# Kernel tuning notes

Hardware: AMD Instinct MI355X
Metric: run time of the kernel (lower is better)

The kernel has to match this reference:

```python
import jax, jax.numpy as jnp
import numpy as np

E, H, HD = 2048, 32, 64
SCALE = HD ** -0.5


def setup_inputs() -> dict:
    key = jax.random.key(0)
    ks = jax.random.split(key, 11)
    B, T, P = 16, 4, 4096
    S = P + T
    return {
        "hidden_states": jax.random.normal(ks[0], (B, T, E), jnp.float32),
        "past_key": jax.random.normal(ks[1], (1, H, P, HD), jnp.float32),
        "past_value": jax.random.normal(ks[2], (1, H, P, HD), jnp.float32),
        "attention_mask": jnp.zeros((B, 1, T, S), jnp.float32),
        "Wq": jax.random.normal(ks[3], (E, E), jnp.float32) * 0.02,
        "bq": jax.random.normal(ks[4], (E,), jnp.float32) * 0.02,
        "Wk": jax.random.normal(ks[5], (E, E), jnp.float32) * 0.02,
        "bk": jax.random.normal(ks[6], (E,), jnp.float32) * 0.02,
        "Wv": jax.random.normal(ks[7], (E, E), jnp.float32) * 0.02,
        "bv": jax.random.normal(ks[8], (E,), jnp.float32) * 0.02,
        "Wo": jax.random.normal(ks[9], (E, E), jnp.float32) * 0.02,
        "bo": jax.random.normal(ks[10], (E,), jnp.float32) * 0.02,
    }


def _shape(x, B, S):
    # [B,S,E] -> [B,H,S,hd]
    return x.reshape(B, S, H, HD).transpose(0, 2, 1, 3)


def reference(hidden_states, past_key, past_value, attention_mask,
              Wq, bq, Wk, bk, Wv, bv, Wo, bo):
    B, T, _ = hidden_states.shape
    # projections (torch Linear: x @ W.T + b); query pre-scaled
    q = _shape(hidden_states @ Wq.T + bq, B, T) * SCALE   # [B,H,T,hd]
    k_new = _shape(hidden_states @ Wk.T + bk, B, T)       # [B,H,T,hd]
    v_new = _shape(hidden_states @ Wv.T + bv, B, T)
    # cache stored with batch 1, broadcast (torch repeat) to B, then concat
    k_past = jnp.broadcast_to(past_key, (B,) + past_key.shape[1:])
    v_past = jnp.broadcast_to(past_value, (B,) + past_value.shape[1:])
    k = jnp.concatenate([k_past, k_new], axis=2)          # [B,H,S,hd]
    v = jnp.concatenate([v_past, v_new], axis=2)
    scores = jnp.einsum('bhtd,bhsd->bhts', q, k)          # [B,H,T,S]
    scores = scores + attention_mask                      # mask is [B,1,T,S]
    scores = jnp.maximum(scores, jnp.finfo(scores.dtype).min)
    w = jax.nn.softmax(scores, axis=-1)
    out = jnp.einsum('bhts,bhsd->bhtd', w, v)             # [B,H,T,hd]
    out = out.transpose(0, 2, 1, 3).reshape(B, T, E)
    return out @ Wo.T + bo
```

## Files before the change

kernel.cpp:

```cpp
#include <hip/hip_runtime.h>


typedef float f4 __attribute__((ext_vector_type(4)));
typedef short s8v __attribute__((ext_vector_type(8)));

#define NEG_HUGE (-3.402823466e38f)

__device__ inline unsigned short f2bs(float x) {
  union { float f; unsigned int u; } a; a.f = x;
  unsigned int u = a.u;
  u += 0x7fffu + ((u >> 16) & 1u);
  return (unsigned short)(u >> 16);
}
__device__ inline float bs2f(unsigned short s) {
  union { unsigned int u; float f; } a; a.u = ((unsigned int)s) << 16;
  return a.f;
}
__device__ inline unsigned long long pack4(float a, float b, float c, float d) {
  return (unsigned long long)f2bs(a) | ((unsigned long long)f2bs(b) << 16)
       | ((unsigned long long)f2bs(c) << 32) | ((unsigned long long)f2bs(d) << 48);
}
__device__ inline s8v cvt8(f4 a, f4 b) {
  s8v r;
  r[0]=(short)f2bs(a[0]); r[1]=(short)f2bs(a[1]); r[2]=(short)f2bs(a[2]); r[3]=(short)f2bs(a[3]);
  r[4]=(short)f2bs(b[0]); r[5]=(short)f2bs(b[1]); r[6]=(short)f2bs(b[2]); r[7]=(short)f2bs(b[3]);
  return r;
}
__device__ inline f4 mfma16(s8v a, s8v b, f4 c) {
  return __builtin_amdgcn_mfma_f32_16x16x32_bf16(a, b, c, 0, 0, 0);
}
__device__ inline f4 fzero() { f4 z = {0.f,0.f,0.f,0.f}; return z; }
__device__ inline float wave_sum(float v) {
  #pragma unroll
  for (int off = 32; off; off >>= 1) v += __shfl_xor(v, off, 64);
  return v;
}

__global__ __launch_bounds__(256) void k_qkv(
    const float* __restrict__ hs, const float* __restrict__ Wq,
    const float* __restrict__ Wk, const float* __restrict__ Wv,
    float* __restrict__ part) {
  __shared__ __align__(16) unsigned short As[64 * 264];
  const int n0 = blockIdx.x * 64;
  const int ksb = blockIdx.y;
  const int p = n0 >> 11;
  const int c0 = n0 & 2047;
  const float* W = (p == 0) ? Wq : (p == 1) ? Wk : Wv;
  const int t = threadIdx.x, lane = t & 63, w = t >> 6;
  const int cl = lane & 15, quad = lane >> 4;

  f4 acc[4];
  #pragma unroll
  for (int i = 0; i < 4; ++i) acc[i] = fzero();

  const int cw = c0 + w * 16 + cl;
  for (int kt = 0; kt < 2; ++kt) {
    const int k0 = ksb * 512 + kt * 256;
    __syncthreads();
    #pragma unroll
    for (int i = 0; i < 16; ++i) {
      int idx4 = t + (i << 8);
      int row = idx4 >> 6;
      int col = (idx4 & 63) << 2;
      f4 v = *reinterpret_cast<const f4*>(hs + row * 2048 + k0 + col);
      *reinterpret_cast<unsigned long long*>(&As[row * 264 + col]) =
          pack4(v[0], v[1], v[2], v[3]);
    }
    __syncthreads();
    const float* wbase = W + (size_t)cw * 2048 + k0;
    #pragma unroll
    for (int ks2 = 0; ks2 < 8; ++ks2) {
      const int kb = ks2 * 32 + quad * 8;
      f4 w0 = *reinterpret_cast<const f4*>(wbase + kb);
      f4 w1 = *reinterpret_cast<const f4*>(wbase + kb + 4);
      s8v bf = cvt8(w0, w1);
      #pragma unroll
      for (int mt = 0; mt < 4; ++mt) {
        s8v af = *reinterpret_cast<const s8v*>(&As[(mt * 16 + cl) * 264 + kb]);
        acc[mt] = mfma16(af, bf, acc[mt]);
      }
    }
  }
  float* outp = part + (size_t)ksb * 64 * 6144;
  #pragma unroll
  for (int mt = 0; mt < 4; ++mt)
    #pragma unroll
    for (int rg = 0; rg < 4; ++rg) {
      int r = mt * 16 + quad * 4 + rg;
      outp[r * 6144 + n0 + w * 16 + cl] = acc[mt][rg];
    }
}

__global__ __launch_bounds__(256) void k_qkv_red(
    const float* __restrict__ part, const float* __restrict__ bq,
    const float* __restrict__ bk, const float* __restrict__ bv,
    unsigned short* __restrict__ qws, float* __restrict__ knew,
    float* __restrict__ vnew) {
  int idx = blockIdx.x * 256 + threadIdx.x;
  int r = idx / 6144;
  int n = idx - r * 6144;
  float s = part[idx] + part[idx + 393216] + part[idx + 786432] + part[idx + 1179648];
  int c = n & 2047, p = n >> 11;
  int h = c >> 6, d = c & 63;
  int b = r >> 2, tt = r & 3;
  if (p == 0) {
    s = (s + bq[c]) * 0.125f;
    qws[h * 4608 + r * 72 + d] = f2bs(s);
  } else if (p == 1) {
    knew[((h * 16 + b) * 4 + tt) * 64 + d] = s + bk[c];
  } else {
    vnew[((h * 16 + b) * 4 + tt) * 64 + d] = s + bv[c];
  }
}

__global__ __launch_bounds__(256) void k_flash(
    const unsigned short* __restrict__ qws, const float* __restrict__ Kp,
    const float* __restrict__ Vp, const float* __restrict__ mask,
    float* __restrict__ Opart, float* __restrict__ mpart,
    float* __restrict__ lpart) {
  __shared__ __align__(16) unsigned short Qs[64 * 72];
  __shared__ __align__(16) float SC[64 * 260];
  __shared__ float mrow[64];
  __shared__ float red[256];
  const int bx = blockIdx.x;
  const int h = bx & 31, cch = bx >> 5;
  const int s0 = cch * 256;
  const int t = threadIdx.x, lane = t & 63, w = t >> 6;
  const int cl = lane & 15, quad = lane >> 4;
  const float* Kh = Kp + (size_t)h * 4096 * 64;
  const float* Vh = Vp + (size_t)h * 4096 * 64;

  {
    const uint4* s4 = reinterpret_cast<const uint4*>(qws + h * 4608);
    uint4* d4 = reinterpret_cast<uint4*>(Qs);
    for (int i = t; i < 576; i += 256) d4[i] = s4[i];
  }
  __syncthreads();

  s8v afr[4][2];
  #pragma unroll
  for (int mt = 0; mt < 4; ++mt)
    #pragma unroll
    for (int k2 = 0; k2 < 2; ++k2)
      afr[mt][k2] = *reinterpret_cast<const s8v*>(
          &Qs[(mt * 16 + cl) * 72 + k2 * 32 + quad * 8]);

  #pragma unroll
  for (int ni = 0; ni < 4; ++ni) {
    const int nt = w * 4 + ni;
    const int srow = s0 + nt * 16 + cl;
    const float* kr = Kh + (size_t)srow * 64 + quad * 8;
    f4 qa[4];
    #pragma unroll
    for (int mt = 0; mt < 4; ++mt) qa[mt] = fzero();
    #pragma unroll
    for (int k2 = 0; k2 < 2; ++k2) {
      f4 k0v = *reinterpret_cast<const f4*>(kr + k2 * 32);
      f4 k1v = *reinterpret_cast<const f4*>(kr + k2 * 32 + 4);
      s8v bf = cvt8(k0v, k1v);
      #pragma unroll
      for (int mt = 0; mt < 4; ++mt) qa[mt] = mfma16(afr[mt][k2], bf, qa[mt]);
    }
    #pragma unroll
    for (int mt = 0; mt < 4; ++mt)
      #pragma unroll
      for (int rg = 0; rg < 4; ++rg) {
        int r = mt * 16 + quad * 4 + rg;
        int sl = nt * 16 + cl;
        float v = qa[mt][rg] + mask[(size_t)r * 4100 + s0 + sl];
        SC[r * 260 + sl] = fmaxf(v, NEG_HUGE);
      }
  }
  __syncthreads();

  {
    const int r = lane, base = w * 64;
    float mx = NEG_HUGE;
    #pragma unroll
    for (int j = 0; j < 64; j += 4) {
      f4 v = *reinterpret_cast<const f4*>(&SC[r * 260 + base + j]);
      mx = fmaxf(fmaxf(fmaxf(mx, v[0]), v[1]), fmaxf(v[2], v[3]));
    }
    red[w * 64 + r] = mx;
  }
  __syncthreads();
  if (t < 64) {
    float m = fmaxf(fmaxf(red[t], red[64 + t]), fmaxf(red[128 + t], red[192 + t]));
    mrow[t] = m;
    mpart[(h * 16 + cch) * 64 + t] = m;
  }
  __syncthreads();
  {
    const int r = lane, base = w * 64;
    const float m = mrow[r];
    float sum = 0.f;
    #pragma unroll
    for (int j = 0; j < 64; j += 4) {
      f4 v = *reinterpret_cast<f4*>(&SC[r * 260 + base + j]);
      f4 e;
      e[0] = __expf(v[0] - m); e[1] = __expf(v[1] - m);
      e[2] = __expf(v[2] - m); e[3] = __expf(v[3] - m);
      *reinterpret_cast<f4*>(&SC[r * 260 + base + j]) = e;
      sum += e[0] + e[1] + e[2] + e[3];
    }
    red[w * 64 + r] = sum;
  }
  __syncthreads();
  if (t < 64)
    lpart[(h * 16 + cch) * 64 + t] = red[t] + red[64 + t] + red[128 + t] + red[192 + t];
  __syncthreads();

  f4 oacc[4];
  #pragma unroll
  for (int mt = 0; mt < 4; ++mt) oacc[mt] = fzero();
  const int dcol = w * 16 + cl;
  #pragma unroll
  for (int k2 = 0; k2 < 8; ++k2) {
    const int sb = k2 * 32 + quad * 8;
    s8v bf;
    #pragma unroll
    for (int j = 0; j < 8; ++j)
      bf[j] = (short)f2bs(Vh[(size_t)(s0 + sb + j) * 64 + dcol]);
    #pragma unroll
    for (int mt = 0; mt < 4; ++mt) {
      const int row = mt * 16 + cl;
      f4 p0 = *reinterpret_cast<const f4*>(&SC[row * 260 + sb]);
      f4 p1 = *reinterpret_cast<const f4*>(&SC[row * 260 + sb + 4]);
      oacc[mt] = mfma16(cvt8(p0, p1), bf, oacc[mt]);
    }
  }
  float* ob = Opart + (size_t)(h * 16 + cch) * 64 * 64;
  #pragma unroll
  for (int mt = 0; mt < 4; ++mt)
    #pragma unroll
    for (int rg = 0; rg < 4; ++rg) {
      int r = mt * 16 + quad * 4 + rg;
      ob[r * 64 + dcol] = oacc[mt][rg];
    }
}

__global__ __launch_bounds__(64) void k_merge(
    const unsigned short* __restrict__ qws, const float* __restrict__ knew,
    const float* __restrict__ vnew, const float* __restrict__ mask,
    const float* __restrict__ Opart, const float* __restrict__ mpart,
    const float* __restrict__ lpart, unsigned short* __restrict__ attn) {
  const int bx = blockIdx.x;
  const int h = bx & 31, b = bx >> 5;
  const int d = threadIdx.x;
  for (int tt = 0; tt < 4; ++tt) {
    const int r = b * 4 + tt;
    float qd = bs2f(qws[h * 4608 + r * 72 + d]);
    float scn[4];
    #pragma unroll
    for (int tp = 0; tp < 4; ++tp) {
      float kn = knew[((h * 16 + b) * 4 + tp) * 64 + d];
      float s = wave_sum(qd * kn);
      s += mask[(size_t)r * 4100 + 4096 + tp];
      scn[tp] = fmaxf(s, NEG_HUGE);
    }
    float mi[16], li[16];
    float mtot = NEG_HUGE;
    #pragma unroll
    for (int i = 0; i < 16; ++i) {
      mi[i] = mpart[(h * 16 + i) * 64 + r];
      li[i] = lpart[(h * 16 + i) * 64 + r];
      mtot = fmaxf(mtot, mi[i]);
    }
    #pragma unroll
    for (int tp = 0; tp < 4; ++tp) mtot = fmaxf(mtot, scn[tp]);
    float ltot = 0.f, od = 0.f;
    #pragma unroll
    for (int i = 0; i < 16; ++i) {
      float fct = __expf(mi[i] - mtot);
      ltot += li[i] * fct;
      od += Opart[((size_t)(h * 16 + i) * 64 + r) * 64 + d] * fct;
    }
    #pragma unroll
    for (int tp = 0; tp < 4; ++tp) {
      float e = __expf(scn[tp] - mtot);
      ltot += e;
      od += e * vnew[((h * 16 + b) * 4 + tp) * 64 + d];
    }
    attn[(size_t)r * 2048 + h * 64 + d] = f2bs(od / ltot);
  }
}

__global__ __launch_bounds__(256) void k_out(
    const unsigned short* __restrict__ attn, const float* __restrict__ Wo,
    float* __restrict__ part) {
  __shared__ __align__(16) unsigned short As[64 * 264];
  const int n0 = blockIdx.x * 64;
  const int ksb = blockIdx.y;
  const int k0 = ksb * 256;
  const int t = threadIdx.x, lane = t & 63, w = t >> 6;
  const int cl = lane & 15, quad = lane >> 4;
  #pragma unroll
  for (int i = 0; i < 8; ++i) {
    int idx8 = t + (i << 8);
    int row = idx8 >> 5;
    int col = (idx8 & 31) << 3;
    *reinterpret_cast<uint4*>(&As[row * 264 + col]) =
        *reinterpret_cast<const uint4*>(attn + (size_t)row * 2048 + k0 + col);
  }
  __syncthreads();
  f4 acc[4];
  #pragma unroll
  for (int i = 0; i < 4; ++i) acc[i] = fzero();
  const int cw = n0 + w * 16 + cl;
  const float* wbase = Wo + (size_t)cw * 2048 + k0;
  #pragma unroll
  for (int ks2 = 0; ks2 < 8; ++ks2) {
    const int kb = ks2 * 32 + quad * 8;
    f4 w0 = *reinterpret_cast<const f4*>(wbase + kb);
    f4 w1 = *reinterpret_cast<const f4*>(wbase + kb + 4);
    s8v bf = cvt8(w0, w1);
    #pragma unroll
    for (int mt = 0; mt < 4; ++mt) {
      s8v af = *reinterpret_cast<const s8v*>(&As[(mt * 16 + cl) * 264 + kb]);
      acc[mt] = mfma16(af, bf, acc[mt]);
    }
  }
  float* op = part + (size_t)ksb * 64 * 2048;
  #pragma unroll
  for (int mt = 0; mt < 4; ++mt)
    #pragma unroll
    for (int rg = 0; rg < 4; ++rg) {
      int r = mt * 16 + quad * 4 + rg;
      op[r * 2048 + n0 + w * 16 + cl] = acc[mt][rg];
    }
}

__global__ __launch_bounds__(256) void k_out_red(
    const float* __restrict__ part, const float* __restrict__ bo,
    float* __restrict__ out) {
  int idx = blockIdx.x * 256 + threadIdx.x;
  int n = idx & 2047;
  float s = bo[n];
  #pragma unroll
  for (int ks = 0; ks < 8; ++ks) s += part[idx + ks * 131072];
  out[idx] = s;
}

extern "C" void kernel_launch(void* const* d_in, const int* in_sizes, int n_in,
                              void* d_out, int out_size, void* d_ws, size_t ws_size,
                              hipStream_t stream) {
  const float* hs   = (const float*)d_in[0];
  const float* pk   = (const float*)d_in[1];
  const float* pv   = (const float*)d_in[2];
  const float* mask = (const float*)d_in[3];
  const float* Wq   = (const float*)d_in[4];
  const float* bq   = (const float*)d_in[5];
  const float* Wk   = (const float*)d_in[6];
  const float* bk   = (const float*)d_in[7];
  const float* Wv   = (const float*)d_in[8];
  const float* bv   = (const float*)d_in[9];
  const float* Wo   = (const float*)d_in[10];
  const float* bo   = (const float*)d_in[11];

  float* f = (float*)d_ws;
  float* qkv_part = f;
  float* o_part   = qkv_part + 1572864;
  float* Opart    = o_part   + 1048576;
  float* mpart    = Opart    + 2097152;
  float* lpart    = mpart    + 32768;
  float* knew     = lpart    + 32768;
  float* vnew     = knew     + 131072;
  unsigned short* qws  = (unsigned short*)(vnew + 131072);
  unsigned short* attn = qws + 147456;

  k_qkv<<<dim3(96, 4), 256, 0, stream>>>(hs, Wq, Wk, Wv, qkv_part);
  k_qkv_red<<<1536, 256, 0, stream>>>(qkv_part, bq, bk, bv, qws, knew, vnew);
  k_flash<<<512, 256, 0, stream>>>(qws, pk, pv, mask, Opart, mpart, lpart);
  k_merge<<<512, 64, 0, stream>>>(qws, knew, vnew, mask, Opart, mpart, lpart, attn);
  k_out<<<dim3(32, 8), 256, 0, stream>>>(attn, Wo, o_part);
  k_out_red<<<512, 256, 0, stream>>>(o_part, bo, (float*)d_out);
}
```

Baseline: 213.3 us.

## Fuse split-K reductions into projection GEMMs and rework flash kernel staging

New measurement: 249.8 us. +17.1%, slower.

```diff
diff --git a/kernel.cpp b/kernel.cpp
--- a/kernel.cpp
+++ b/kernel.cpp
@@ -16,10 +16,6 @@
   union { unsigned int u; float f; } a; a.u = ((unsigned int)s) << 16;
   return a.f;
 }
-__device__ inline unsigned long long pack4(float a, float b, float c, float d) {
-  return (unsigned long long)f2bs(a) | ((unsigned long long)f2bs(b) << 16)
-       | ((unsigned long long)f2bs(c) << 32) | ((unsigned long long)f2bs(d) << 48);
-}
 __device__ inline s8v cvt8(f4 a, f4 b) {
   s8v r;
   r[0]=(short)f2bs(a[0]); r[1]=(short)f2bs(a[1]); r[2]=(short)f2bs(a[2]); r[3]=(short)f2bs(a[3]);
@@ -36,80 +32,45 @@
   return v;
 }
 
-__global__ __launch_bounds__(256) void k_qkv(
+__global__ __launch_bounds__(256) void k_qkvp(
     const float* __restrict__ hs, const float* __restrict__ Wq,
     const float* __restrict__ Wk, const float* __restrict__ Wv,
-    float* __restrict__ part) {
-  __shared__ __align__(16) unsigned short As[64 * 264];
-  const int n0 = blockIdx.x * 64;
-  const int ksb = blockIdx.y;
+    const float* __restrict__ bq, const float* __restrict__ bk,
+    const float* __restrict__ bv, unsigned short* __restrict__ qws,
+    float* __restrict__ knew, float* __restrict__ vnew) {
+  const int n0 = blockIdx.x * 16;
   const int p = n0 >> 11;
   const int c0 = n0 & 2047;
   const float* W = (p == 0) ? Wq : (p == 1) ? Wk : Wv;
+  const float* bias = (p == 0) ? bq : (p == 1) ? bk : bv;
   const int t = threadIdx.x, lane = t & 63, w = t >> 6;
-  const int cl = lane & 15, quad = lane >> 4;
-
-  f4 acc[4];
-  #pragma unroll
-  for (int i = 0; i < 4; ++i) acc[i] = fzero();
-
-  const int cw = c0 + w * 16 + cl;
-  for (int kt = 0; kt < 2; ++kt) {
-    const int k0 = ksb * 512 + kt * 256;
-    __syncthreads();
-    #pragma unroll
-    for (int i = 0; i < 16; ++i) {
-      int idx4 = t + (i << 8);
-      int row = idx4 >> 6;
-      int col = (idx4 & 63) << 2;
-      f4 v = *reinterpret_cast<const f4*>(hs + row * 2048 + k0 + col);
-      *reinterpret_cast<unsigned long long*>(&As[row * 264 + col]) =
-          pack4(v[0], v[1], v[2], v[3]);
-    }
-    __syncthreads();
-    const float* wbase = W + (size_t)cw * 2048 + k0;
-    #pragma unroll
-    for (int ks2 = 0; ks2 < 8; ++ks2) {
-      const int kb = ks2 * 32 + quad * 8;
-      f4 w0 = *reinterpret_cast<const f4*>(wbase + kb);
-      f4 w1 = *reinterpret_cast<const f4*>(wbase + kb + 4);
-      s8v bf = cvt8(w0, w1);
-      #pragma unroll
-      for (int mt = 0; mt < 4; ++mt) {
-        s8v af = *reinterpret_cast<const s8v*>(&As[(mt * 16 + cl) * 264 + kb]);
-        acc[mt] = mfma16(af, bf, acc[mt]);
-      }
-    }
-  }
-  float* outp = part + (size_t)ksb * 64 * 6144;
-  #pragma unroll
-  for (int mt = 0; mt < 4; ++mt)
-    #pragma unroll
-    for (int rg = 0; rg < 4; ++rg) {
-      int r = mt * 16 + quad * 4 + rg;
-      outp[r * 6144 + n0 + w * 16 + cl] = acc[mt][rg];
-    }
-}
-
-__global__ __launch_bounds__(256) void k_qkv_red(
-    const float* __restrict__ part, const float* __restrict__ bq,
-    const float* __restrict__ bk, const float* __restrict__ bv,
-    unsigned short* __restrict__ qws, float* __restrict__ knew,
-    float* __restrict__ vnew) {
-  int idx = blockIdx.x * 256 + threadIdx.x;
-  int r = idx / 6144;
-  int n = idx - r * 6144;
-  float s = part[idx] + part[idx + 393216] + part[idx + 786432] + part[idx + 1179648];
-  int c = n & 2047, p = n >> 11;
-  int h = c >> 6, d = c & 63;
-  int b = r >> 2, tt = r & 3;
-  if (p == 0) {
-    s = (s + bq[c]) * 0.125f;
-    qws[h * 4608 + r * 72 + d] = f2bs(s);
-  } else if (p == 1) {
-    knew[((h * 16 + b) * 4 + tt) * 64 + d] = s + bk[c];
-  } else {
-    vnew[((h * 16 + b) * 4 + tt) * 64 + d] = s + bv[c];
+  const int cl = lane & 15, q = lane >> 4;
+
+  const float* arow = hs + (size_t)(w * 16 + cl) * 2048 + q * 8;
+  const float* brow = W + (size_t)(c0 + cl) * 2048 + q * 8;
+
+  f4 acc = fzero();
+  #pragma unroll 8
+  for (int k0 = 0; k0 < 2048; k0 += 32) {
+    f4 a0 = *reinterpret_cast<const f4*>(arow + k0);
+    f4 a1 = *reinterpret_cast<const f4*>(arow + k0 + 4);
+    f4 b0 = *reinterpret_cast<const f4*>(brow + k0);
+    f4 b1 = *reinterpret_cast<const f4*>(brow + k0 + 4);
+    acc = mfma16(cvt8(a0, a1), cvt8(b0, b1), acc);
+  }
+  const int c = c0 + cl, h = c >> 6, d = c & 63;
+  #pragma unroll
+  for (int rg = 0; rg < 4; ++rg) {
+    const int r = w * 16 + q * 4 + rg;
+    const int b = r >> 2, tt = r & 3;
+    float v = acc[rg] + bias[c];
+    if (p == 0) {
+      qws[h * 4608 + r * 72 + d] = f2bs(v * 0.125f);
+    } else if (p == 1) {
+      knew[((h * 16 + b) * 4 + tt) * 64 + d] = v;
+    } else {
+      vnew[((h * 16 + b) * 4 + tt) * 64 + d] = v;
+    }
   }
 }
 
@@ -118,24 +79,32 @@
     const float* __restrict__ Vp, const float* __restrict__ mask,
     float* __restrict__ Opart, float* __restrict__ mpart,
     float* __restrict__ lpart) {
-  __shared__ __align__(16) unsigned short Qs[64 * 72];
-  __shared__ __align__(16) float SC[64 * 260];
+  __shared__ __align__(16) unsigned short Pb[64 * 264];
+  __shared__ __align__(16) unsigned short Vb[256 * 74];
   __shared__ float mrow[64];
-  __shared__ float red[256];
+  __shared__ float psum[4][64];
+  float* tmp = reinterpret_cast<float*>(Pb);
+  float* s2  = reinterpret_cast<float*>(Pb) + 64 * 68;
+
   const int bx = blockIdx.x;
   const int h = bx & 31, cch = bx >> 5;
   const int s0 = cch * 256;
   const int t = threadIdx.x, lane = t & 63, w = t >> 6;
-  const int cl = lane & 15, quad = lane >> 4;
+  const int cl = lane & 15, q = lane >> 4;
   const float* Kh = Kp + (size_t)h * 4096 * 64;
   const float* Vh = Vp + (size_t)h * 4096 * 64;
 
-  {
-    const uint4* s4 = reinterpret_cast<const uint4*>(qws + h * 4608);
-    uint4* d4 = reinterpret_cast<uint4*>(Qs);
-    for (int i = t; i < 576; i += 256) d4[i] = s4[i];
-  }
-  __syncthreads();
+  unsigned int* Vb32 = reinterpret_cast<unsigned int*>(Vb);
+  #pragma unroll
+  for (int i = 0; i < 16; ++i) {
+    int idx = t + i * 256;
+    int s = idx >> 4, d4 = (idx & 15) << 2;
+    f4 v = *reinterpret_cast<const f4*>(Vh + (size_t)(s0 + s) * 64 + d4);
+    unsigned int lo = (unsigned int)f2bs(v[0]) | ((unsigned int)f2bs(v[1]) << 16);
+    unsigned int hi = (unsigned int)f2bs(v[2]) | ((unsigned int)f2bs(v[3]) << 16);
+    int u = s * 37 + (d4 >> 1);
+    Vb32[u] = lo; Vb32[u + 1] = hi;
+  }
 
   s8v afr[4][2];
   #pragma unroll
@@ -143,202 +112,188 @@
     #pragma unroll
     for (int k2 = 0; k2 < 2; ++k2)
       afr[mt][k2] = *reinterpret_cast<const s8v*>(
-          &Qs[(mt * 16 + cl) * 72 + k2 * 32 + quad * 8]);
-
+          qws + h * 4608 + (mt * 16 + cl) * 72 + k2 * 32 + q * 8);
+
+  f4 sc[4][4];
+  #pragma unroll
+  for (int ni = 0; ni < 4; ++ni)
+    #pragma unroll
+    for (int mt = 0; mt < 4; ++mt) sc[ni][mt] = fzero();
   #pragma unroll
   for (int ni = 0; ni < 4; ++ni) {
-    const int nt = w * 4 + ni;
-    const int srow = s0 + nt * 16 + cl;
-    const float* kr = Kh + (size_t)srow * 64 + quad * 8;
-    f4 qa[4];
-    #pragma unroll
-    for (int mt = 0; mt < 4; ++mt) qa[mt] = fzero();
+    const int srow = s0 + (w * 4 + ni) * 16 + cl;
+    const float* kr = Kh + (size_t)srow * 64 + q * 8;
     #pragma unroll
     for (int k2 = 0; k2 < 2; ++k2) {
       f4 k0v = *reinterpret_cast<const f4*>(kr + k2 * 32);
       f4 k1v = *reinterpret_cast<const f4*>(kr + k2 * 32 + 4);
       s8v bf = cvt8(k0v, k1v);
       #pragma unroll
-      for (int mt = 0; mt < 4; ++mt) qa[mt] = mfma16(afr[mt][k2], bf, qa[mt]);
-    }
-    #pragma unroll
-    for (int mt = 0; mt < 4; ++mt)
+      for (int mt = 0; mt < 4; ++mt)
+        sc[ni][mt] = mfma16(afr[mt][k2], bf, sc[ni][mt]);
+    }
+  }
+  #pragma unroll
+  for (int mt = 0; mt < 4; ++mt)
+    #pragma unroll
+    for (int rg = 0; rg < 4; ++rg) {
+      const int r = mt * 16 + q * 4 + rg;
+      float mx = NEG_HUGE;
       #pragma unroll
-      for (int rg = 0; rg < 4; ++rg) {
-        int r = mt * 16 + quad * 4 + rg;
-        int sl = nt * 16 + cl;
-        float v = qa[mt][rg] + mask[(size_t)r * 4100 + s0 + sl];
-        SC[r * 260 + sl] = fmaxf(v, NEG_HUGE);
+      for (int ni = 0; ni < 4; ++ni) {
+        const int col = s0 + (w * 4 + ni) * 16 + cl;
+        float v = sc[ni][mt][rg] + mask[(size_t)r * 4100 + col];
+        v = fmaxf(v, NEG_HUGE);
+        sc[ni][mt][rg] = v;
+        mx = fmaxf(mx, v);
       }
-  }
-  __syncthreads();
-
+      tmp[r * 68 + w * 16 + cl] = mx;
+    }
+  __syncthreads();
   {
-    const int r = lane, base = w * 64;
-    float mx = NEG_HUGE;
-    #pragma unroll
-    for (int j = 0; j < 64; j += 4) {
-      f4 v = *reinterpret_cast<const f4*>(&SC[r * 260 + base + j]);
-      mx = fmaxf(fmaxf(fmaxf(mx, v[0]), v[1]), fmaxf(v[2], v[3]));
-    }
-    red[w * 64 + r] = mx;
+    const int row = t >> 2, qt = t & 3;
+    const float* tr = tmp + row * 68 + qt * 16;
+    float m = fmaxf(fmaxf(tr[0], tr[1]), fmaxf(tr[2], tr[3]));
+    #pragma unroll
+    for (int j = 4; j < 16; j += 4)
+      m = fmaxf(m, fmaxf(fmaxf(tr[j], tr[j+1]), fmaxf(tr[j+2], tr[j+3])));
+    s2[row * 4 + qt] = m;
   }
   __syncthreads();
   if (t < 64) {
-    float m = fmaxf(fmaxf(red[t], red[64 + t]), fmaxf(red[128 + t], red[192 + t]));
+    float m = fmaxf(fmaxf(s2[t*4], s2[t*4+1]), fmaxf(s2[t*4+2], s2[t*4+3]));
     mrow[t] = m;
     mpart[(h * 16 + cch) * 64 + t] = m;
   }
   __syncthreads();
+  #pragma unroll
+  for (int mt = 0; mt < 4; ++mt)
+    #pragma unroll
+    for (int rg = 0; rg < 4; ++rg) {
+      const int r = mt * 16 + q * 4 + rg;
+      const float m = mrow[r];
+      #pragma unroll
+      for (int ni = 0; ni < 4; ++ni) {
+        float e = __expf(sc[ni][mt][rg] - m);
+        Pb[r * 264 + (w * 4 + ni) * 16 + cl] = f2bs(e);
+      }
+    }
+  __syncthreads();
   {
-    const int r = lane, base = w * 64;
-    const float m = mrow[r];
-    float sum = 0.f;
-    #pragma unroll
-    for (int j = 0; j < 64; j += 4) {
-      f4 v = *reinterpret_cast<f4*>(&SC[r * 260 + base + j]);
-      f4 e;
-      e[0] = __expf(v[0] - m); e[1] = __expf(v[1] - m);
-      e[2] = __expf(v[2] - m); e[3] = __expf(v[3] - m);
-      *reinterpret_cast<f4*>(&SC[r * 260 + base + j]) = e;
-      sum += e[0] + e[1] + e[2] + e[3];
-    }
-    red[w * 64 + r] = sum;
-  }
-  __syncthreads();
-  if (t < 64)
-    lpart[(h * 16 + cch) * 64 + t] = red[t] + red[64 + t] + red[128 + t] + red[192 + t];
-  __syncthreads();
-
+    const int r = t & 63, qt = t >> 6;
+    float s = 0.f;
+    #pragma unroll
+    for (int j8 = 0; j8 < 8; ++j8) {
+      const unsigned short* pp = &Pb[r * 264 + qt * 64 + j8 * 8];
+      #pragma unroll
+      for (int j = 0; j < 8; ++j) s += bs2f(pp[j]);
+    }
+    psum[qt][r] = s;
+  }
   f4 oacc[4];
   #pragma unroll
   for (int mt = 0; mt < 4; ++mt) oacc[mt] = fzero();
   const int dcol = w * 16 + cl;
   #pragma unroll
   for (int k2 = 0; k2 < 8; ++k2) {
-    const int sb = k2 * 32 + quad * 8;
+    const int sb = k2 * 32 + q * 8;
     s8v bf;
     #pragma unroll
-    for (int j = 0; j < 8; ++j)
-      bf[j] = (short)f2bs(Vh[(size_t)(s0 + sb + j) * 64 + dcol]);
+    for (int j = 0; j < 8; ++j) bf[j] = (short)Vb[(sb + j) * 74 + dcol];
     #pragma unroll
     for (int mt = 0; mt < 4; ++mt) {
-      const int row = mt * 16 + cl;
-      f4 p0 = *reinterpret_cast<const f4*>(&SC[row * 260 + sb]);
-      f4 p1 = *reinterpret_cast<const f4*>(&SC[row * 260 + sb + 4]);
-      oacc[mt] = mfma16(cvt8(p0, p1), bf, oacc[mt]);
-    }
-  }
+      s8v pa = *reinterpret_cast<const s8v*>(&Pb[(mt * 16 + cl) * 264 + sb]);
+      oacc[mt] = mfma16(pa, bf, oacc[mt]);
+    }
+  }
+  __syncthreads();
+  if (t < 64)
+    lpart[(h * 16 + cch) * 64 + t] = psum[0][t] + psum[1][t] + psum[2][t] + psum[3][t];
   float* ob = Opart + (size_t)(h * 16 + cch) * 64 * 64;
   #pragma unroll
   for (int mt = 0; mt < 4; ++mt)
     #pragma unroll
-    for (int rg = 0; rg < 4; ++rg) {
-      int r = mt * 16 + quad * 4 + rg;
-      ob[r * 64 + dcol] = oacc[mt][rg];
-    }
-}
-
-__global__ __launch_bounds__(64) void k_merge(
+    for (int rg = 0; rg < 4; ++rg)
+      ob[(mt * 16 + q * 4 + rg) * 64 + dcol] = oacc[mt][rg];
+}
+
+__global__ __launch_bounds__(256) void k_merge(
     const unsigned short* __restrict__ qws, const float* __restrict__ knew,
     const float* __restrict__ vnew, const float* __restrict__ mask,
     const float* __restrict__ Opart, const float* __restrict__ mpart,
     const float* __restrict__ lpart, unsigned short* __restrict__ attn) {
   const int bx = blockIdx.x;
   const int h = bx & 31, b = bx >> 5;
-  const int d = threadIdx.x;
-  for (int tt = 0; tt < 4; ++tt) {
-    const int r = b * 4 + tt;
-    float qd = bs2f(qws[h * 4608 + r * 72 + d]);
-    float scn[4];
-    #pragma unroll
-    for (int tp = 0; tp < 4; ++tp) {
-      float kn = knew[((h * 16 + b) * 4 + tp) * 64 + d];
-      float s = wave_sum(qd * kn);
-      s += mask[(size_t)r * 4100 + 4096 + tp];
-      scn[tp] = fmaxf(s, NEG_HUGE);
-    }
-    float mi[16], li[16];
-    float mtot = NEG_HUGE;
-    #pragma unroll
-    for (int i = 0; i < 16; ++i) {
-      mi[i] = mpart[(h * 16 + i) * 64 + r];
-      li[i] = lpart[(h * 16 + i) * 64 + r];
-      mtot = fmaxf(mtot, mi[i]);
-    }
-    #pragma unroll
-    for (int tp = 0; tp < 4; ++tp) mtot = fmaxf(mtot, scn[tp]);
-    float ltot = 0.f, od = 0.f;
-    #pragma unroll
-    for (int i = 0; i < 16; ++i) {
-      float fct = __expf(mi[i] - mtot);
-      ltot += li[i] * fct;
-      od += Opart[((size_t)(h * 16 + i) * 64 + r) * 64 + d] * fct;
-    }
-    #pragma unroll
-    for (int tp = 0; tp < 4; ++tp) {
-      float e = __expf(scn[tp] - mtot);
-      ltot += e;
-      od += e * vnew[((h * 16 + b) * 4 + tp) * 64 + d];
-    }
-    attn[(size_t)r * 2048 + h * 64 + d] = f2bs(od / ltot);
-  }
-}
-
-__global__ __launch_bounds__(256) void k_out(
+  const int d = threadIdx.x & 63, tt = threadIdx.x >> 6;
+  const int r = b * 4 + tt;
+  float qd = bs2f(qws[h * 4608 + r * 72 + d]);
+  float scn[4];
+  #pragma unroll
+  for (int tp = 0; tp < 4; ++tp) {
+    float kn = knew[((h * 16 + b) * 4 + tp) * 64 + d];
+    float s = wave_sum(qd * kn);
+    s += mask[(size_t)r * 4100 + 4096 + tp];
+    scn[tp] = fmaxf(s, NEG_HUGE);
+  }
+  float mi[16], li[16];
+  float mtot = NEG_HUGE;
+  #pragma unroll
+  for (int i = 0; i < 16; ++i) {
+    mi[i] = mpart[(h * 16 + i) * 64 + r];
+    li[i] = lpart[(h * 16 + i) * 64 + r];
+    mtot = fmaxf(mtot, mi[i]);
+  }
+  #pragma unroll
+  for (int tp = 0; tp < 4; ++tp) mtot = fmaxf(mtot, scn[tp]);
+  float ltot = 0.f, od = 0.f;
+  #pragma unroll
+  for (int i = 0; i < 16; ++i) {
+    float fct = __expf(mi[i] - mtot);
+    ltot += li[i] * fct;
+    od += Opart[((size_t)(h * 16 + i) * 64 + r) * 64 + d] * fct;
+  }
+  #pragma unroll
+  for (int tp = 0; tp < 4; ++tp) {
+    float e = __expf(scn[tp] - mtot);
+    ltot += e;
+    od += e * vnew[((h * 16 + b) * 4 + tp) * 64 + d];
+  }
+  attn[(size_t)r * 2048 + h * 64 + d] = f2bs(od / ltot);
+}
+
+__global__ __launch_bounds__(512) void k_out(
     const unsigned short* __restrict__ attn, const float* __restrict__ Wo,
-    float* __restrict__ part) {
-  __shared__ __align__(16) unsigned short As[64 * 264];
-  const int n0 = blockIdx.x * 64;
-  const int ksb = blockIdx.y;
-  const int k0 = ksb * 256;
+    const float* __restrict__ bo, float* __restrict__ out) {
+  __shared__ float red[4][16][17];
+  const int n0 = blockIdx.x * 16;
   const int t = threadIdx.x, lane = t & 63, w = t >> 6;
-  const int cl = lane & 15, quad = lane >> 4;
-  #pragma unroll
-  for (int i = 0; i < 8; ++i) {
-    int idx8 = t + (i << 8);
-    int row = idx8 >> 5;
-    int col = (idx8 & 31) << 3;
-    *reinterpret_cast<uint4*>(&As[row * 264 + col]) =
-        *reinterpret_cast<const uint4*>(attn + (size_t)row * 2048 + k0 + col);
-  }
-  __syncthreads();
-  f4 acc[4];
-  #pragma unroll
-  for (int i = 0; i < 4; ++i) acc[i] = fzero();
-  const int cw = n0 + w * 16 + cl;
-  const float* wbase = Wo + (size_t)cw * 2048 + k0;
-  #pragma unroll
-  for (int ks2 = 0; ks2 < 8; ++ks2) {
-    const int kb = ks2 * 32 + quad * 8;
-    f4 w0 = *reinterpret_cast<const f4*>(wbase + kb);
-    f4 w1 = *reinterpret_cast<const f4*>(wbase + kb + 4);
-    s8v bf = cvt8(w0, w1);
-    #pragma unroll
-    for (int mt = 0; mt < 4; ++mt) {
-      s8v af = *reinterpret_cast<const s8v*>(&As[(mt * 16 + cl) * 264 + kb]);
-      acc[mt] = mfma16(af, bf, acc[mt]);
-    }
-  }
-  float* op = part + (size_t)ksb * 64 * 2048;
-  #pragma unroll
-  for (int mt = 0; mt < 4; ++mt)
+  const int mt = w & 3, kh = w >> 2;
+  const int cl = lane & 15, q = lane >> 4;
+  const unsigned short* arow = attn + (size_t)(mt * 16 + cl) * 2048;
+  const float* brow = Wo + (size_t)(n0 + cl) * 2048;
+  f4 acc = fzero();
+  const int kb = kh * 1024 + q * 8;
+  #pragma unroll 8
+  for (int step = 0; step < 32; ++step) {
+    const int k = kb + step * 32;
+    s8v af = *reinterpret_cast<const s8v*>(arow + k);
+    f4 b0 = *reinterpret_cast<const f4*>(brow + k);
+    f4 b1 = *reinterpret_cast<const f4*>(brow + k + 4);
+    acc = mfma16(af, cvt8(b0, b1), acc);
+  }
+  if (kh == 1) {
+    #pragma unroll
+    for (int rg = 0; rg < 4; ++rg) red[mt][q * 4 + rg][cl] = acc[rg];
+  }
+  __syncthreads();
+  if (kh == 0) {
+    const int c = n0 + cl;
     #pragma unroll
     for (int rg = 0; rg < 4; ++rg) {
-      int r = mt * 16 + quad * 4 + rg;
-      op[r * 2048 + n0 + w * 16 + cl] = acc[mt][rg];
-    }
-}
-
-__global__ __launch_bounds__(256) void k_out_red(
-    const float* __restrict__ part, const float* __restrict__ bo,
-    float* __restrict__ out) {
-  int idx = blockIdx.x * 256 + threadIdx.x;
-  int n = idx & 2047;
-  float s = bo[n];
-  #pragma unroll
-  for (int ks = 0; ks < 8; ++ks) s += part[idx + ks * 131072];
-  out[idx] = s;
+      const int r = mt * 16 + q * 4 + rg;
+      out[(size_t)r * 2048 + c] = acc[rg] + red[mt][q * 4 + rg][cl] + bo[c];
+    }
+  }
 }
 
 extern "C" void kernel_launch(void* const* d_in, const int* in_sizes, int n_in,
@@ -358,20 +313,16 @@
   const float* bo   = (const float*)d_in[11];
 
   float* f = (float*)d_ws;
-  float* qkv_part = f;
-  float* o_part   = qkv_part + 1572864;
-  float* Opart    = o_part   + 1048576;
-  float* mpart    = Opart    + 2097152;
-  float* lpart    = mpart    + 32768;
-  float* knew     = lpart    + 32768;
-  float* vnew     = knew     + 131072;
+  float* Opart = f;
+  float* mpart = Opart + 2097152;
+  float* lpart = mpart + 32768;
+  float* knew  = lpart + 32768;
+  float* vnew  = knew + 131072;
   unsigned short* qws  = (unsigned short*)(vnew + 131072);
   unsigned short* attn = qws + 147456;
 
-  k_qkv<<<dim3(96, 4), 256, 0, stream>>>(hs, Wq, Wk, Wv, qkv_part);
-  k_qkv_red<<<1536, 256, 0, stream>>>(qkv_part, bq, bk, bv, qws, knew, vnew);
+  k_qkvp<<<384, 256, 0, stream>>>(hs, Wq, Wk, Wv, bq, bk, bv, qws, knew, vnew);
   k_flash<<<512, 256, 0, stream>>>(qws, pk, pv, mask, Opart, mpart, lpart);
-  k_merge<<<512, 64, 0, stream>>>(qws, knew, vnew, mask, Opart, mpart, lpart, attn);
-  k_out<<<dim3(32, 8), 256, 0, stream>>>(attn, Wo, o_part);
-  k_out_red<<<512, 256, 0, stream>>>(o_part, bo, (float*)d_out);
-}
+  k_merge<<<512, 256, 0, stream>>>(qws, knew, vnew, mask, Opart, mpart, lpart, attn);
+  k_out<<<128, 512, 0, stream>>>(attn, Wo, bo, (float*)d_out);
+}
```
